# Kernel optimization log

Measured on AMD Instinct MI355X. Metric: run time of the kernel, lower is better.

## Reference

```python
import jax, jax.numpy as jnp
import numpy as np

ALPHA = 0.2  # LeakyReLU negative slope
NEG = -9e15


def _gat_heads(x, adj_mask, W, a):
    # x: (B,N,F); W: (H,F,O); a: (H,2O); adj_mask: (B,N,N) bool
    O = W.shape[-1]
    Wh = jnp.einsum('bnf,hfo->bhno', x, W)            # (B,H,N,O)
    e1 = jnp.einsum('bhno,ho->bhn', Wh, a[:, :O])     # Wh @ a[:O]
    e2 = jnp.einsum('bhno,ho->bhn', Wh, a[:, O:])     # Wh @ a[O:]
    e = jax.nn.leaky_relu(e1[:, :, :, None] + e2[:, :, None, :], ALPHA)  # (B,H,N,N)
    e = jnp.where(adj_mask[:, None], e, NEG)
    attn = jax.nn.softmax(e, axis=-1)
    return jnp.einsum('bhnm,bhmo->bhno', attn, Wh)    # (B,H,N,O)


def _gat_block(x, adj_mask, non_pad_mask, W_heads, a_heads, W_out, a_out):
    # multi-head layer, concat=True -> elu per head, then concat on feature dim
    h = jax.nn.elu(_gat_heads(x, adj_mask, W_heads, a_heads))  # (B,H,N,O)
    B, H, N, O = h.shape
    h = jnp.transpose(h, (0, 2, 1, 3)).reshape(B, N, H * O)
    h = h * non_pad_mask
    # out layer: single head, concat=False (no inner elu)
    h = _gat_heads(h, adj_mask, W_out[None], a_out[None])[:, 0]  # (B,N,noutput)
    h = h * non_pad_mask
    return jax.nn.elu(h)


def setup_inputs() -> dict:
    key = jax.random.key(0)
    ks = jax.random.split(key, 8)
    B, N = 32, 256
    vocab, F, O, H, OUT = 200, 300, 256, 8, 512
    fea = jax.random.randint(ks[0], (B, N), 0, vocab, dtype=jnp.int32)
    adj = jax.random.randint(ks[1], (B, N, N), 0, 2, dtype=jnp.int32)
    non_pad_mask = jnp.ones((B, N, 1), dtype=jnp.float32)
    embed = jax.random.normal(ks[2], (vocab, F), dtype=jnp.float32)
    W_heads = jax.random.normal(ks[3], (H, F, O), dtype=jnp.float32) / np.sqrt(F)
    a_heads = jax.random.normal(ks[4], (H, 2 * O), dtype=jnp.float32) / np.sqrt(2 * O)
    W_out = jax.random.normal(ks[5], (H * O, OUT), dtype=jnp.float32) / np.sqrt(H * O)
    a_out = jax.random.normal(ks[6], (2 * OUT,), dtype=jnp.float32) / np.sqrt(2 * OUT)
    return {"fea": fea, "adj": adj, "non_pad_mask": non_pad_mask, "embed": embed,
            "W_heads": W_heads, "a_heads": a_heads, "W_out": W_out, "a_out": a_out}


def reference(fea, adj, non_pad_mask, embed, W_heads, a_heads, W_out, a_out):
    adj_mask = adj > 0
    x = embed[fea]  # (B,N,F)
    # GAT_num = 1; dropout is identity in eval mode
    x = _gat_block(x, adj_mask, non_pad_mask, W_heads, a_heads, W_out, a_out)
    return x  # (B, N, 512)
```

## Files before the change

### kernel.cpp

```cpp
#include <hip/hip_runtime.h>
#include <math.h>


typedef _Float16 f16;
typedef __attribute__((ext_vector_type(8))) _Float16 f16x8;
typedef __attribute__((ext_vector_type(4))) _Float16 f16x4;
typedef __attribute__((ext_vector_type(4))) float f32x4;

__device__ __forceinline__ void async16(const void* g, void* lds) {
  __builtin_amdgcn_global_load_lds(
      (const __attribute__((address_space(1))) void*)g,
      (__attribute__((address_space(3))) void*)lds, 16, 0, 0);
}

__global__ void k_prep_x(const int* __restrict__ fea, const float* __restrict__ embed,
                         f16* __restrict__ x16) {
  int row = blockIdx.x;
  int t = threadIdx.x;
  int tok = fea[row];
  float v = (t < 300) ? embed[tok * 300 + t] : 0.f;
  x16[(size_t)row * 320 + t] = (f16)v;
}

__global__ void k_prep_wc(const float* __restrict__ W, f16* __restrict__ WcT) {
  __shared__ float tile[32][33];
  int bx = blockIdx.x, by = blockIdx.y, h = blockIdx.z;
  int tid = threadIdx.x;
  int c = tid & 31, q = tid >> 5;
#pragma unroll
  for (int i = 0; i < 4; ++i) {
    int tt = q + i * 8;
    int t = bx * 32 + tt;
    float v = (t < 300) ? W[((size_t)h * 300 + t) * 256 + by * 32 + c] : 0.f;
    tile[tt][c] = v;
  }
  __syncthreads();
#pragma unroll
  for (int i = 0; i < 4; ++i) {
    int oo = q + i * 8;
    int gc = h * 256 + by * 32 + oo;
    WcT[(size_t)gc * 320 + bx * 32 + c] = (f16)tile[c][oo];
  }
}

__global__ void k_prep_wo(const float* __restrict__ W, f16* __restrict__ WoT) {
  __shared__ float tile[32][33];
  int bx = blockIdx.x, by = blockIdx.y;
  int tid = threadIdx.x;
  int c = tid & 31, q = tid >> 5;
#pragma unroll
  for (int i = 0; i < 4; ++i) {
    int kk = q + i * 8;
    tile[kk][c] = W[((size_t)bx * 32 + kk) * 512 + by * 32 + c];
  }
  __syncthreads();
#pragma unroll
  for (int i = 0; i < 4; ++i) {
    int oo = q + i * 8;
    WoT[((size_t)by * 32 + oo) * 2048 + bx * 32 + c] = (f16)tile[c][oo];
  }
}

template <int KDIM, int NCOLS, int TN, int EDOT>
__global__ __launch_bounds__(256, 4) void k_gemm(const f16* __restrict__ A,
                                                 const f16* __restrict__ BT,
                                                 f16* __restrict__ outT,
                                                 const float* __restrict__ avec,
                                                 float* __restrict__ e1,
                                                 float* __restrict__ e2) {
  __shared__ f16 As[128 * 32];
  __shared__ f16 Bs[TN * 32];
  const int by = blockIdx.x, bx = blockIdx.y;
  const int tid = threadIdx.x;
  const int wave = tid >> 6, lane = tid & 63;
  const int wm = wave >> 1, wn = wave & 1;
  const int lrow = lane & 15, quad = lane >> 4;
  const int srow = lane >> 2;
  const int scol = (lane & 3) * 8;
  constexpr int NT = TN / 32;

  f32x4 acc[4][NT] = {};
  const f16* Ag = A + (size_t)by * 128 * KDIM;
  const f16* Bg = BT + (size_t)bx * TN * KDIM;

  for (int k0 = 0; k0 < KDIM; k0 += 32) {
    __syncthreads();
#pragma unroll
    for (int j = 0; j < 2; ++j) {
      const int r0 = wave * 32 + j * 16;
      async16(Ag + (size_t)(r0 + srow) * KDIM + k0 + scol, &As[r0 * 32]);
    }
#pragma unroll
    for (int j = 0; j < TN / 64; ++j) {
      const int r0 = wave * (TN / 4) + j * 16;
      async16(Bg + (size_t)(r0 + srow) * KDIM + k0 + scol, &Bs[r0 * 32]);
    }
    __syncthreads();
    f16x8 af[4], bf[NT];
#pragma unroll
    for (int t = 0; t < 4; ++t)
      af[t] = *(const f16x8*)&As[(wm * 64 + t * 16 + lrow) * 32 + quad * 8];
#pragma unroll
    for (int t = 0; t < NT; ++t)
      bf[t] = *(const f16x8*)&Bs[(wn * (TN / 2) + t * 16 + lrow) * 32 + quad * 8];
#pragma unroll
    for (int mt = 0; mt < 4; ++mt)
#pragma unroll
      for (int nt = 0; nt < NT; ++nt)
        acc[mt][nt] = __builtin_amdgcn_mfma_f32_16x16x32_f16(af[mt], bf[nt], acc[mt][nt], 0, 0, 0);
  }

  const int b = (by * 128) >> 8;
  const int nbase0 = (by * 128) & 255;
#pragma unroll
  for (int mt = 0; mt < 4; ++mt) {
    const int nb = nbase0 + wm * 64 + mt * 16 + quad * 4;
#pragma unroll
    for (int nt = 0; nt < NT; ++nt) {
      const int gc = bx * TN + wn * (TN / 2) + nt * 16 + lrow;
      f16x4 v;
#pragma unroll
      for (int r = 0; r < 4; ++r) v[r] = (f16)acc[mt][nt][r];
      *(f16x4*)&outT[((size_t)b * NCOLS + gc) * 256 + nb] = v;
    }
  }

  float a1v[NT], a2v[NT];
#pragma unroll
  for (int nt = 0; nt < NT; ++nt) {
    const int gc = bx * TN + wn * (TN / 2) + nt * 16 + lrow;
    if (EDOT == 1) {
      int hh = gc >> 8, oo = gc & 255;
      a1v[nt] = avec[hh * 512 + oo];
      a2v[nt] = avec[hh * 512 + 256 + oo];
    } else {
      a1v[nt] = avec[gc];
      a2v[nt] = avec[NCOLS + gc];
    }
  }
  const int hblk = (EDOT == 1) ? ((bx * TN) >> 8) : 0;
  const int ebase = (EDOT == 1) ? ((b * 8 + hblk) * 256) : (b * 256);
#pragma unroll
  for (int mt = 0; mt < 4; ++mt) {
    float s1[4] = {0.f, 0.f, 0.f, 0.f}, s2[4] = {0.f, 0.f, 0.f, 0.f};
#pragma unroll
    for (int nt = 0; nt < NT; ++nt)
#pragma unroll
      for (int r = 0; r < 4; ++r) {
        s1[r] += acc[mt][nt][r] * a1v[nt];
        s2[r] += acc[mt][nt][r] * a2v[nt];
      }
#pragma unroll
    for (int r = 0; r < 4; ++r)
#pragma unroll
      for (int m = 1; m < 16; m <<= 1) {
        s1[r] += __shfl_xor(s1[r], m);
        s2[r] += __shfl_xor(s2[r], m);
      }
    if (lrow == 0) {
      const int nb = nbase0 + wm * 64 + mt * 16 + quad * 4;
#pragma unroll
      for (int r = 0; r < 4; ++r) {
        atomicAdd(&e1[ebase + nb + r], s1[r]);
        atomicAdd(&e2[ebase + nb + r], s2[r]);
      }
    }
  }
}

#define PSTRIDE 264

__global__ __launch_bounds__(256, 4) void k_attn1(
    const f16* __restrict__ WhT, const float* __restrict__ e1g, const float* __restrict__ e2g,
    const int* __restrict__ adj, const float* __restrict__ npm, f16* __restrict__ h1) {
  int h = blockIdx.x, b = blockIdx.y, nt0 = blockIdx.z;
  int bh = b * 8 + h;
  int n0 = nt0 * 64;
  __shared__ f16 P[64 * PSTRIDE];
  int tid = threadIdx.x;
  int wave = tid >> 6, lane = tid & 63;

  float4 e2v = *(const float4*)&e2g[bh * 256 + lane * 4];
  float e2m = fmaxf(fmaxf(e2v.x, e2v.y), fmaxf(e2v.z, e2v.w));
#pragma unroll
  for (int m = 1; m < 64; m <<= 1) e2m = fmaxf(e2m, __shfl_xor(e2m, m));
#pragma unroll 4
  for (int i = 0; i < 16; ++i) {
    int row = i * 4 + wave;
    int gn = b * 256 + n0 + row;
    float er = e1g[bh * 256 + n0 + row];
    float sh = er + e2m;
    sh = sh > 0.f ? sh : 0.2f * sh;
    int4 aj = *(const int4*)&adj[(size_t)gn * 256 + lane * 4];
    float p0, p1, p2, p3;
    {
      float v = er + e2v.x; v = v > 0.f ? v : 0.2f * v;
      p0 = aj.x ? __expf(v - sh) : 0.f;
      v = er + e2v.y; v = v > 0.f ? v : 0.2f * v;
      p1 = aj.y ? __expf(v - sh) : 0.f;
      v = er + e2v.z; v = v > 0.f ? v : 0.2f * v;
      p2 = aj.z ? __expf(v - sh) : 0.f;
      v = er + e2v.w; v = v > 0.f ? v : 0.2f * v;
      p3 = aj.w ? __expf(v - sh) : 0.f;
    }
    float sm = p0 + p1 + p2 + p3;
#pragma unroll
    for (int m = 1; m < 64; m <<= 1) sm += __shfl_xor(sm, m);
    float rs = 1.f / sm;
    f16x4 pw;
    pw[0] = (f16)(p0 * rs); pw[1] = (f16)(p1 * rs);
    pw[2] = (f16)(p2 * rs); pw[3] = (f16)(p3 * rs);
    *(f16x4*)&P[row * PSTRIDE + lane * 4] = pw;
  }
  __syncthreads();

  int lrow = lane & 15, quad = lane >> 4;
  f32x4 acc[4][4] = {};
  const f16* Ag = WhT + (size_t)bh * 65536;
#pragma unroll 2
  for (int k0 = 0; k0 < 256; k0 += 32) {
    f16x8 af[4], bf[4];
#pragma unroll
    for (int mt = 0; mt < 4; ++mt)
      af[mt] = *(const f16x8*)&Ag[(size_t)(wave * 64 + mt * 16 + lrow) * 256 + k0 + quad * 8];
#pragma unroll
    for (int nt = 0; nt < 4; ++nt)
      bf[nt] = *(const f16x8*)&P[(nt * 16 + lrow) * PSTRIDE + k0 + quad * 8];
#pragma unroll
    for (int mt = 0; mt < 4; ++mt)
#pragma unroll
      for (int nt = 0; nt < 4; ++nt)
        acc[mt][nt] = __builtin_amdgcn_mfma_f32_16x16x32_f16(af[mt], bf[nt], acc[mt][nt], 0, 0, 0);
  }
#pragma unroll
  for (int nt = 0; nt < 4; ++nt) {
    int nloc = nt * 16 + lrow;
    int gn = b * 256 + n0 + nloc;
    float pm = npm[gn];
#pragma unroll
    for (int mt = 0; mt < 4; ++mt) {
      int o0 = wave * 64 + mt * 16 + quad * 4;
      f16x4 st;
#pragma unroll
      for (int r = 0; r < 4; ++r) {
        float v = acc[mt][nt][r];
        v = v > 0.f ? v : (__expf(v) - 1.f);
        st[r] = (f16)(v * pm);
      }
      *(f16x4*)&h1[(size_t)gn * 2048 + h * 256 + o0] = st;
    }
  }
}

__global__ __launch_bounds__(256, 4) void k_attn2(
    const f16* __restrict__ Wh2T, const float* __restrict__ e1g, const float* __restrict__ e2g,
    const int* __restrict__ adj, const float* __restrict__ npm, float* __restrict__ out) {
  int oh = blockIdx.x, b = blockIdx.y, nt0 = blockIdx.z;
  int n0 = nt0 * 64;
  __shared__ f16 P[64 * PSTRIDE];
  int tid = threadIdx.x;
  int wave = tid >> 6, lane = tid & 63;

  float4 e2v = *(const float4*)&e2g[b * 256 + lane * 4];
  float e2m = fmaxf(fmaxf(e2v.x, e2v.y), fmaxf(e2v.z, e2v.w));
#pragma unroll
  for (int m = 1; m < 64; m <<= 1) e2m = fmaxf(e2m, __shfl_xor(e2m, m));
#pragma unroll 4
  for (int i = 0; i < 16; ++i) {
    int row = i * 4 + wave;
    int gn = b * 256 + n0 + row;
    float er = e1g[b * 256 + n0 + row];
    float sh = er + e2m;
    sh = sh > 0.f ? sh : 0.2f * sh;
    int4 aj = *(const int4*)&adj[(size_t)gn * 256 + lane * 4];
    float p0, p1, p2, p3;
    {
      float v = er + e2v.x; v = v > 0.f ? v : 0.2f * v;
      p0 = aj.x ? __expf(v - sh) : 0.f;
      v = er + e2v.y; v = v > 0.f ? v : 0.2f * v;
      p1 = aj.y ? __expf(v - sh) : 0.f;
      v = er + e2v.z; v = v > 0.f ? v : 0.2f * v;
      p2 = aj.z ? __expf(v - sh) : 0.f;
      v = er + e2v.w; v = v > 0.f ? v : 0.2f * v;
      p3 = aj.w ? __expf(v - sh) : 0.f;
    }
    float sm = p0 + p1 + p2 + p3;
#pragma unroll
    for (int m = 1; m < 64; m <<= 1) sm += __shfl_xor(sm, m);
    float rs = 1.f / sm;
    f16x4 pw;
    pw[0] = (f16)(p0 * rs); pw[1] = (f16)(p1 * rs);
    pw[2] = (f16)(p2 * rs); pw[3] = (f16)(p3 * rs);
    *(f16x4*)&P[row * PSTRIDE + lane * 4] = pw;
  }
  __syncthreads();

  int lrow = lane & 15, quad = lane >> 4;
  f32x4 acc[4][4] = {};
  const f16* Ag = Wh2T + (size_t)b * 512 * 256 + (size_t)oh * 65536;
#pragma unroll 2
  for (int k0 = 0; k0 < 256; k0 += 32) {
    f16x8 af[4], bf[4];
#pragma unroll
    for (int mt = 0; mt < 4; ++mt)
      af[mt] = *(const f16x8*)&Ag[(size_t)(wave * 64 + mt * 16 + lrow) * 256 + k0 + quad * 8];
#pragma unroll
    for (int nt = 0; nt < 4; ++nt)
      bf[nt] = *(const f16x8*)&P[(nt * 16 + lrow) * PSTRIDE + k0 + quad * 8];
#pragma unroll
    for (int mt = 0; mt < 4; ++mt)
#pragma unroll
      for (int nt = 0; nt < 4; ++nt)
        acc[mt][nt] = __builtin_amdgcn_mfma_f32_16x16x32_f16(af[mt], bf[nt], acc[mt][nt], 0, 0, 0);
  }
#pragma unroll
  for (int nt = 0; nt < 4; ++nt) {
    int nloc = nt * 16 + lrow;
    int gn = b * 256 + n0 + nloc;
    float pm = npm[gn];
#pragma unroll
    for (int mt = 0; mt < 4; ++mt) {
      int o0 = oh * 256 + wave * 64 + mt * 16 + quad * 4;
      float4 st;
      float v0 = acc[mt][nt][0] * pm;
      float v1 = acc[mt][nt][1] * pm;
      float v2 = acc[mt][nt][2] * pm;
      float v3 = acc[mt][nt][3] * pm;
      st.x = v0 > 0.f ? v0 : (__expf(v0) - 1.f);
      st.y = v1 > 0.f ? v1 : (__expf(v1) - 1.f);
      st.z = v2 > 0.f ? v2 : (__expf(v2) - 1.f);
      st.w = v3 > 0.f ? v3 : (__expf(v3) - 1.f);
      *(float4*)&out[(size_t)gn * 512 + o0] = st;
    }
  }
}

extern "C" void kernel_launch(void* const* d_in, const int* in_sizes, int n_in,
                              void* d_out, int out_size, void* d_ws, size_t ws_size,
                              hipStream_t stream) {
  (void)in_sizes; (void)n_in; (void)out_size; (void)ws_size;
  const int*   fea   = (const int*)d_in[0];
  const int*   adj   = (const int*)d_in[1];
  const float* npm   = (const float*)d_in[2];
  const float* embed = (const float*)d_in[3];
  const float* Whd   = (const float*)d_in[4];
  const float* ah    = (const float*)d_in[5];
  const float* Wo    = (const float*)d_in[6];
  const float* ao    = (const float*)d_in[7];
  float* out = (float*)d_out;

  char* ws = (char*)d_ws;
  f16* x16  = (f16*)ws;  ws += (size_t)8192 * 320 * 2;
  f16* WcT  = (f16*)ws;  ws += (size_t)2048 * 320 * 2;
  f16* WoT  = (f16*)ws;  ws += (size_t)512 * 2048 * 2;
  f16* WhT  = (f16*)ws;  ws += (size_t)32 * 8 * 256 * 256 * 2;
  f16* h1   = (f16*)ws;  ws += (size_t)8192 * 2048 * 2;
  f16* Wh2T = (f16*)ws;  ws += (size_t)32 * 512 * 256 * 2;
  float* e1  = (float*)ws; ws += (size_t)65536 * 4;
  float* e2  = (float*)ws; ws += (size_t)65536 * 4;
  float* e12 = (float*)ws; ws += (size_t)8192 * 4;
  float* e22 = (float*)ws; ws += (size_t)8192 * 4;

  hipMemsetAsync(e1, 0, ((size_t)65536 * 2 + 8192 * 2) * 4, stream);

  k_prep_x<<<8192, 320, 0, stream>>>(fea, embed, x16);
  k_prep_wc<<<dim3(10, 8, 8), 256, 0, stream>>>(Whd, WcT);
  k_prep_wo<<<dim3(64, 16), 256, 0, stream>>>(Wo, WoT);

  k_gemm<320, 2048, 128, 1><<<dim3(64, 16), 256, 0, stream>>>(x16, WcT, WhT, ah, e1, e2);
  k_attn1<<<dim3(8, 32, 4), 256, 0, stream>>>(WhT, e1, e2, adj, npm, h1);

  k_gemm<2048, 512, 64, 2><<<dim3(64, 8), 256, 0, stream>>>(h1, WoT, Wh2T, ao, e12, e22);
  k_attn2<<<dim3(2, 32, 4), 256, 0, stream>>>(Wh2T, e12, e22, adj, npm, out);
}
```

Measured before the change: 205.7 us.

## Split-K second GAT GEMM with atomic fp32 accumulation and XOR-swizzled LDS tiles

The second projection GEMM (K=2048) becomes a split-K kernel over four K chunks with 128x128 tiles. Partial sums are atomically added into an fp32 buffer, and a new combine kernel converts them to fp16 and computes the attention dot products. Both GEMMs also gain an XOR swizzle on the LDS layout to reduce bank conflicts. The aim is more blocks for the long-K GEMM and cheaper LDS reads, at the cost of an extra 16MB memset, many fp32 atomics and an extra kernel pass.

```diff
diff --git a/kernel.cpp b/kernel.cpp
--- a/kernel.cpp
+++ b/kernel.cpp
@@ -61,27 +61,27 @@
   }
 }
 
-template <int KDIM, int NCOLS, int TN, int EDOT>
-__global__ __launch_bounds__(256, 4) void k_gemm(const f16* __restrict__ A,
-                                                 const f16* __restrict__ BT,
-                                                 f16* __restrict__ outT,
-                                                 const float* __restrict__ avec,
-                                                 float* __restrict__ e1,
-                                                 float* __restrict__ e2) {
+template <int KDIM, int NCOLS>
+__global__ __launch_bounds__(256, 4) void k_gemm1(const f16* __restrict__ A,
+                                                  const f16* __restrict__ BT,
+                                                  f16* __restrict__ outT,
+                                                  const float* __restrict__ avec,
+                                                  float* __restrict__ e1,
+                                                  float* __restrict__ e2) {
   __shared__ f16 As[128 * 32];
-  __shared__ f16 Bs[TN * 32];
+  __shared__ f16 Bs[128 * 32];
   const int by = blockIdx.x, bx = blockIdx.y;
   const int tid = threadIdx.x;
   const int wave = tid >> 6, lane = tid & 63;
   const int wm = wave >> 1, wn = wave & 1;
   const int lrow = lane & 15, quad = lane >> 4;
   const int srow = lane >> 2;
-  const int scol = (lane & 3) * 8;
-  constexpr int NT = TN / 32;
-
-  f32x4 acc[4][NT] = {};
+  const int scol = ((lane & 3) ^ ((lane >> 3) & 3)) * 8;
+  const int sq = (quad ^ ((lrow >> 1) & 3)) * 8;
+
+  f32x4 acc[4][4] = {};
   const f16* Ag = A + (size_t)by * 128 * KDIM;
-  const f16* Bg = BT + (size_t)bx * TN * KDIM;
+  const f16* Bg = BT + (size_t)bx * 128 * KDIM;
 
   for (int k0 = 0; k0 < KDIM; k0 += 32) {
     __syncthreads();
@@ -89,24 +89,19 @@
     for (int j = 0; j < 2; ++j) {
       const int r0 = wave * 32 + j * 16;
       async16(Ag + (size_t)(r0 + srow) * KDIM + k0 + scol, &As[r0 * 32]);
-    }
-#pragma unroll
-    for (int j = 0; j < TN / 64; ++j) {
-      const int r0 = wave * (TN / 4) + j * 16;
       async16(Bg + (size_t)(r0 + srow) * KDIM + k0 + scol, &Bs[r0 * 32]);
     }
     __syncthreads();
-    f16x8 af[4], bf[NT];
-#pragma unroll
-    for (int t = 0; t < 4; ++t)
-      af[t] = *(const f16x8*)&As[(wm * 64 + t * 16 + lrow) * 32 + quad * 8];
-#pragma unroll
-    for (int t = 0; t < NT; ++t)
-      bf[t] = *(const f16x8*)&Bs[(wn * (TN / 2) + t * 16 + lrow) * 32 + quad * 8];
-#pragma unroll
-    for (int mt = 0; mt < 4; ++mt)
-#pragma unroll
-      for (int nt = 0; nt < NT; ++nt)
+    f16x8 af[4], bf[4];
+#pragma unroll
+    for (int t = 0; t < 4; ++t) {
+      af[t] = *(const f16x8*)&As[(wm * 64 + t * 16 + lrow) * 32 + sq];
+      bf[t] = *(const f16x8*)&Bs[(wn * 64 + t * 16 + lrow) * 32 + sq];
+    }
+#pragma unroll
+    for (int mt = 0; mt < 4; ++mt)
+#pragma unroll
+      for (int nt = 0; nt < 4; ++nt)
         acc[mt][nt] = __builtin_amdgcn_mfma_f32_16x16x32_f16(af[mt], bf[nt], acc[mt][nt], 0, 0, 0);
   }
 
@@ -116,8 +111,8 @@
   for (int mt = 0; mt < 4; ++mt) {
     const int nb = nbase0 + wm * 64 + mt * 16 + quad * 4;
 #pragma unroll
-    for (int nt = 0; nt < NT; ++nt) {
-      const int gc = bx * TN + wn * (TN / 2) + nt * 16 + lrow;
+    for (int nt = 0; nt < 4; ++nt) {
+      const int gc = bx * 128 + wn * 64 + nt * 16 + lrow;
       f16x4 v;
 #pragma unroll
       for (int r = 0; r < 4; ++r) v[r] = (f16)acc[mt][nt][r];
@@ -125,26 +120,21 @@
     }
   }
 
-  float a1v[NT], a2v[NT];
-#pragma unroll
-  for (int nt = 0; nt < NT; ++nt) {
-    const int gc = bx * TN + wn * (TN / 2) + nt * 16 + lrow;
-    if (EDOT == 1) {
-      int hh = gc >> 8, oo = gc & 255;
-      a1v[nt] = avec[hh * 512 + oo];
-      a2v[nt] = avec[hh * 512 + 256 + oo];
-    } else {
-      a1v[nt] = avec[gc];
-      a2v[nt] = avec[NCOLS + gc];
-    }
-  }
-  const int hblk = (EDOT == 1) ? ((bx * TN) >> 8) : 0;
-  const int ebase = (EDOT == 1) ? ((b * 8 + hblk) * 256) : (b * 256);
+  float a1v[4], a2v[4];
+#pragma unroll
+  for (int nt = 0; nt < 4; ++nt) {
+    const int gc = bx * 128 + wn * 64 + nt * 16 + lrow;
+    int hh = gc >> 8, oo = gc & 255;
+    a1v[nt] = avec[hh * 512 + oo];
+    a2v[nt] = avec[hh * 512 + 256 + oo];
+  }
+  const int hblk = (bx * 128) >> 8;
+  const int ebase = (b * 8 + hblk) * 256;
 #pragma unroll
   for (int mt = 0; mt < 4; ++mt) {
     float s1[4] = {0.f, 0.f, 0.f, 0.f}, s2[4] = {0.f, 0.f, 0.f, 0.f};
 #pragma unroll
-    for (int nt = 0; nt < NT; ++nt)
+    for (int nt = 0; nt < 4; ++nt)
 #pragma unroll
       for (int r = 0; r < 4; ++r) {
         s1[r] += acc[mt][nt][r] * a1v[nt];
@@ -166,6 +156,83 @@
       }
     }
   }
+}
+
+__global__ __launch_bounds__(256, 4) void k_gemm_sk(const f16* __restrict__ A,
+                                                    const f16* __restrict__ BT,
+                                                    float* __restrict__ acc32) {
+  __shared__ f16 As[128 * 32];
+  __shared__ f16 Bs[128 * 32];
+  const int by = blockIdx.x, bx = blockIdx.y, kz = blockIdx.z;
+  const int tid = threadIdx.x;
+  const int wave = tid >> 6, lane = tid & 63;
+  const int wm = wave >> 1, wn = wave & 1;
+  const int lrow = lane & 15, quad = lane >> 4;
+  const int srow = lane >> 2;
+  const int scol = ((lane & 3) ^ ((lane >> 3) & 3)) * 8;
+  const int sq = (quad ^ ((lrow >> 1) & 3)) * 8;
+
+  f32x4 acc[4][4] = {};
+  const f16* Ag = A + (size_t)by * 128 * 2048;
+  const f16* Bg = BT + (size_t)bx * 128 * 2048;
+  const int kbeg = kz * 512;
+
+  for (int k0 = kbeg; k0 < kbeg + 512; k0 += 32) {
+    __syncthreads();
+#pragma unroll
+    for (int j = 0; j < 2; ++j) {
+      const int r0 = wave * 32 + j * 16;
+      async16(Ag + (size_t)(r0 + srow) * 2048 + k0 + scol, &As[r0 * 32]);
+      async16(Bg + (size_t)(r0 + srow) * 2048 + k0 + scol, &Bs[r0 * 32]);
+    }
+    __syncthreads();
+    f16x8 af[4], bf[4];
+#pragma unroll
+    for (int t = 0; t < 4; ++t) {
+      af[t] = *(const f16x8*)&As[(wm * 64 + t * 16 + lrow) * 32 + sq];
+      bf[t] = *(const f16x8*)&Bs[(wn * 64 + t * 16 + lrow) * 32 + sq];
+    }
+#pragma unroll
+    for (int mt = 0; mt < 4; ++mt)
+#pragma unroll
+      for (int nt = 0; nt < 4; ++nt)
+        acc[mt][nt] = __builtin_amdgcn_mfma_f32_16x16x32_f16(af[mt], bf[nt], acc[mt][nt], 0, 0, 0);
+  }
+
+  const int b = (by * 128) >> 8;
+  const int nbase0 = (by * 128) & 255;
+#pragma unroll
+  for (int mt = 0; mt < 4; ++mt) {
+    const int nb = nbase0 + wm * 64 + mt * 16 + quad * 4;
+#pragma unroll
+    for (int nt = 0; nt < 4; ++nt) {
+      const int gc = bx * 128 + wn * 64 + nt * 16 + lrow;
+      float* dst = &acc32[((size_t)b * 512 + gc) * 256 + nb];
+#pragma unroll
+      for (int r = 0; r < 4; ++r) atomicAdd(dst + r, acc[mt][nt][r]);
+    }
+  }
+}
+
+__global__ void k_comb(const float* __restrict__ acc32, const float* __restrict__ ao,
+                       f16* __restrict__ Wh2T, float* __restrict__ e12,
+                       float* __restrict__ e22) {
+  int oc = blockIdx.x;
+  int b = blockIdx.y;
+  int n = threadIdx.x;
+  const float* base = acc32 + ((size_t)b * 512 + oc * 64) * 256 + n;
+  f16* wbase = Wh2T + ((size_t)b * 512 + oc * 64) * 256 + n;
+  float s1 = 0.f, s2 = 0.f;
+#pragma unroll 8
+  for (int j = 0; j < 64; ++j) {
+    float v = base[(size_t)j * 256];
+    int o2 = oc * 64 + j;
+    s1 += v * ao[o2];
+    s2 += v * ao[512 + o2];
+    wbase[(size_t)j * 256] = (f16)v;
+  }
+  atomicAdd(&e12[b * 256 + n], s1);
+  atomicAdd(&e22[b * 256 + n], s2);
 }
 
 #define PSTRIDE 264
@@ -356,20 +423,23 @@
   f16* WhT  = (f16*)ws;  ws += (size_t)32 * 8 * 256 * 256 * 2;
   f16* h1   = (f16*)ws;  ws += (size_t)8192 * 2048 * 2;
   f16* Wh2T = (f16*)ws;  ws += (size_t)32 * 512 * 256 * 2;
+  float* Wh2acc = (float*)ws; ws += (size_t)32 * 512 * 256 * 4;
   float* e1  = (float*)ws; ws += (size_t)65536 * 4;
   float* e2  = (float*)ws; ws += (size_t)65536 * 4;
   float* e12 = (float*)ws; ws += (size_t)8192 * 4;
   float* e22 = (float*)ws; ws += (size_t)8192 * 4;
 
-  hipMemsetAsync(e1, 0, ((size_t)65536 * 2 + 8192 * 2) * 4, stream);
+  hipMemsetAsync(Wh2acc, 0,
+                 ((size_t)32 * 512 * 256 + 65536 * 2 + 8192 * 2) * 4, stream);
 
   k_prep_x<<<8192, 320, 0, stream>>>(fea, embed, x16);
   k_prep_wc<<<dim3(10, 8, 8), 256, 0, stream>>>(Whd, WcT);
   k_prep_wo<<<dim3(64, 16), 256, 0, stream>>>(Wo, WoT);
 
-  k_gemm<320, 2048, 128, 1><<<dim3(64, 16), 256, 0, stream>>>(x16, WcT, WhT, ah, e1, e2);
+  k_gemm1<320, 2048><<<dim3(64, 16), 256, 0, stream>>>(x16, WcT, WhT, ah, e1, e2);
   k_attn1<<<dim3(8, 32, 4), 256, 0, stream>>>(WhT, e1, e2, adj, npm, h1);
 
-  k_gemm<2048, 512, 64, 2><<<dim3(64, 8), 256, 0, stream>>>(h1, WoT, Wh2T, ao, e12, e22);
+  k_gemm_sk<<<dim3(64, 4, 4), 256, 0, stream>>>(h1, WoT, Wh2acc);
+  k_comb<<<dim3(8, 32), 256, 0, stream>>>(Wh2acc, ao, Wh2T, e12, e22);
   k_attn2<<<dim3(2, 32, 4), 256, 0, stream>>>(Wh2T, e12, e22, adj, npm, out);
 }
```

Result: slower. 397.4 us (+93.1%).
